# Performance work log

Hardware: AMD Instinct MI355X
Metric: run time of the kernel (lower is better)

## Reference

```python
import jax, jax.numpy as jnp
import numpy as np

MAX_PAGES = 4096
KEY_DIM = 64
PAGE_NUMBER_BITS = 20
BATCH = 32768


def setup_inputs() -> dict:
    key = jax.random.key(0)
    ks = jax.random.split(key, 10)
    return {
        "virtual_page_bits": jax.random.uniform(ks[0], (BATCH, PAGE_NUMBER_BITS), dtype=jnp.float32),
        "page_keys": jax.random.normal(ks[1], (MAX_PAGES, KEY_DIM), dtype=jnp.float32) * 0.1,
        "virtual_pages": jax.random.normal(ks[2], (MAX_PAGES, PAGE_NUMBER_BITS), dtype=jnp.float32) * 0.5,
        "physical_pages": jax.random.normal(ks[3], (MAX_PAGES, PAGE_NUMBER_BITS), dtype=jnp.float32) * 0.5,
        "permissions": jax.random.normal(ks[4], (MAX_PAGES, 4), dtype=jnp.float32) * 0.5,
        "W1": jax.random.normal(ks[5], (PAGE_NUMBER_BITS, 2 * KEY_DIM), dtype=jnp.float32) * 0.1,
        "b1": jnp.zeros((2 * KEY_DIM,), dtype=jnp.float32),
        "W2": jax.random.normal(ks[6], (2 * KEY_DIM, KEY_DIM), dtype=jnp.float32) * 0.1,
        "b2": jnp.zeros((KEY_DIM,), dtype=jnp.float32),
        "temperature": jnp.array(0.5, dtype=jnp.float32),
    }


def reference(virtual_page_bits, page_keys, virtual_pages, physical_pages,
              permissions, W1, b1, W2, b2, temperature):
    # query encoder: Linear -> GELU (exact, torch default) -> Linear
    h = jax.nn.gelu(virtual_page_bits @ W1 + b1, approximate=False)
    query = h @ W2 + b2                                  # [B, key_dim]

    stored_virt = jax.nn.sigmoid(virtual_pages)          # [P, 20]
    key_sim = query @ page_keys.T                        # [B, P]

    x2 = jnp.sum(virtual_page_bits ** 2, axis=-1, keepdims=True)   # [B, 1]
    s2 = jnp.sum(stored_virt ** 2, axis=-1)                        # [P]
    cross = virtual_page_bits @ stored_virt.T                      # [B, P]
    page_sim = -(x2 + s2[None, :] - 2.0 * cross)                   # [B, P]

    combined_sim = key_sim + 2.0 * page_sim
    temp = jnp.maximum(jnp.abs(temperature), 0.1)
    attention = jax.nn.softmax(combined_sim / temp, axis=-1)       # [B, P]

    physical_page_bits = attention @ jax.nn.sigmoid(physical_pages)  # [B, 20]
    perms = attention @ jax.nn.sigmoid(permissions)                  # [B, 4]
    return (physical_page_bits, perms[:, 0], perms[:, 1:4])
```

## Files before the change

### kernel.cpp

```cpp
#include <hip/hip_runtime.h>
#include <hip/hip_bf16.h>
#include <math.h>

typedef __attribute__((ext_vector_type(8))) short short8v;
typedef __attribute__((ext_vector_type(4))) short short4v;
typedef __attribute__((ext_vector_type(4))) float float4v;
typedef unsigned short u16;

#define BATCH 32768
#define PAGES 4096
#define QB 64
#define PT 64
#define NT (PAGES / PT)
#define QS_LD 136

__device__ __forceinline__ u16 f2bf(float f) {
  __hip_bfloat16 h = __float2bfloat16(f);
  union { __hip_bfloat16 h; u16 u; } cv; cv.h = h; return cv.u;
}
__device__ __forceinline__ float bf2f(u16 b) {
  union { u16 u; __hip_bfloat16 h; } cv; cv.u = b; return __bfloat162float(cv.h);
}
__device__ __forceinline__ float sigm(float x) { return 1.0f / (1.0f + __expf(-x)); }

__global__ __launch_bounds__(256) void prep_k(const float* __restrict__ pk,
                                              const float* __restrict__ vp,
                                              u16* __restrict__ Kg,
                                              float* __restrict__ cbg) {
  int tg = blockIdx.x * 256 + threadIdx.x;
  int p = tg >> 4, c = tg & 15;
  short8v vals;
#pragma unroll
  for (int e = 0; e < 8; ++e) {
    int d = c * 8 + e;
    u16 bits;
    if (d < 64) {
      bits = f2bf(pk[p * 64 + d]);
    } else if (d < 124) {
      int j = (d - 64) % 20;
      float s4 = 4.0f * sigm(vp[p * 20 + j]);
      u16 hi = f2bf(s4);
      bits = (d < 104) ? hi : f2bf(s4 - bf2f(hi));
    } else {
      bits = 0;
    }
    vals[e] = (short)bits;
  }
  int cs = c ^ (p & 7);
  *reinterpret_cast<short8v*>(&Kg[p * 128 + cs * 8]) = vals;
  if (c == 0) {
    float s2 = 0.0f;
#pragma unroll
    for (int j = 0; j < 20; ++j) { float s = sigm(vp[p * 20 + j]); s2 += s * s; }
    cbg[p] = -2.0f * s2;
  }
}

__global__ __launch_bounds__(256) void prep_v(const float* __restrict__ ph,
                                              const float* __restrict__ pr,
                                              u16* __restrict__ Vtg) {
  int tg = blockIdx.x * 256 + threadIdx.x;
  int p = tg & 4095, v = tg >> 12;
  float x;
  if (v < 20) x = sigm(ph[p * 20 + v]);
  else if (v < 24) x = sigm(pr[p * 4 + (v - 20)]);
  else x = 0.0f;
  int s = (p & 15) * 4 + ((p >> 4) & 3);
  Vtg[v * 4096 + (p & ~63) + s] = f2bf(x);
}

__global__ __launch_bounds__(256) void mmu_main(
    const float* __restrict__ vpb_g, const float* __restrict__ W1g,
    const float* __restrict__ b1g, const float* __restrict__ W2g,
    const float* __restrict__ b2g, const float* __restrict__ temp_g,
    const u16* __restrict__ Kg, const float* __restrict__ cbg,
    const u16* __restrict__ Vtg, float* __restrict__ outp) {
  __shared__ __align__(16) u16 Qs[QB * QS_LD];
  __shared__ __align__(16) float vpb_s[QB * 20];
  __shared__ __align__(16) char un[26624];
  float* W1s = (float*)un;
  float* hs  = (float*)(un + 10240);
  u16* Ks    = (u16*)un;
  u16* Ps    = (u16*)(un + 16384);

  const int tid = threadIdx.x;
  const int q0 = blockIdx.x * QB;

  for (int i = tid; i < QB * 20; i += 256) vpb_s[i] = vpb_g[q0 * 20 + i];
  for (int i = tid; i < 20 * 128; i += 256) W1s[i] = W1g[i];
  __syncthreads();

  for (int i = tid; i < QB * 64; i += 256) {
    int q = i >> 6, c = 64 + (i & 63);
    u16 bits;
    if (c < 84) bits = f2bf(vpb_s[q * 20 + c - 64]);
    else if (c < 104) { float v = vpb_s[q * 20 + c - 84]; u16 hi = f2bf(v); bits = f2bf(v - bf2f(hi)); }
    else if (c < 124) bits = f2bf(vpb_s[q * 20 + c - 104]);
    else bits = 0;
    Qs[q * QS_LD + c] = bits;
  }

  for (int half = 0; half < 2; ++half) {
    const int qb = half * 32;
    for (int i = tid; i < 32 * 128; i += 256) {
      int q = i >> 7, cc = i & 127;
      float acc = b1g[cc];
#pragma unroll
      for (int j = 0; j < 20; ++j) acc += vpb_s[(qb + q) * 20 + j] * W1s[j * 128 + cc];
      hs[i] = 0.5f * acc * (1.0f + erff(acc * 0.70710678118654752f));
    }
    __syncthreads();
    for (int i = tid; i < 32 * 64; i += 256) {
      int q = i >> 6, k = i & 63;
      float acc = b2g[k];
      for (int c = 0; c < 128; ++c) acc += hs[q * 128 + c] * W2g[c * 64 + k];
      Qs[(qb + q) * QS_LD + k] = f2bf(acc);
    }
    __syncthreads();
  }

  const int lane = tid & 63, w = tid >> 6, g = lane >> 4, li = lane & 15;
  const float invt = 1.0f / fmaxf(fabsf(temp_g[0]), 0.1f);
  const float c2 = invt * 1.4426950408889634f;

  short8v qf[4];
#pragma unroll
  for (int ks = 0; ks < 4; ++ks)
    qf[ks] = *reinterpret_cast<const short8v*>(&Qs[(w * 16 + li) * QS_LD + ks * 32 + g * 8]);

  float4v Ov0 = {0.f, 0.f, 0.f, 0.f}, Ov1 = {0.f, 0.f, 0.f, 0.f};
  float m_run[4] = {-1e30f, -1e30f, -1e30f, -1e30f};
  float lsum[4] = {0.f, 0.f, 0.f, 0.f};
  u16* Psw = Ps + w * (16 * 72);

  for (int t = 0; t < NT; ++t) {
    const short8v* gsrc = reinterpret_cast<const short8v*>(Kg) + t * 1024;
    short8v s0 = gsrc[tid], s1 = gsrc[256 + tid], s2 = gsrc[512 + tid], s3 = gsrc[768 + tid];
    __syncthreads();
    short8v* kdst = reinterpret_cast<short8v*>(Ks);
    kdst[tid] = s0; kdst[256 + tid] = s1; kdst[512 + tid] = s2; kdst[768 + tid] = s3;
    __syncthreads();

    const int p0 = t * PT;
    float sv[4][4];
#pragma unroll
    for (int ct = 0; ct < 4; ++ct) {
      float4v acc = {0.f, 0.f, 0.f, 0.f};
      const int row = ct * 16 + li;
      const float cbv = cbg[p0 + row];
#pragma unroll
      for (int ks = 0; ks < 4; ++ks) {
        const int ch = (ks * 4 + g) ^ (row & 7);
        short8v b = *reinterpret_cast<const short8v*>(&Ks[row * 128 + ch * 8]);
        acc = __builtin_amdgcn_mfma_f32_16x16x32_bf16(qf[ks], b, acc, 0, 0, 0);
      }
#pragma unroll
      for (int r = 0; r < 4; ++r) sv[ct][r] = acc[r] + cbv;
    }

    float mt[4];
#pragma unroll
    for (int r = 0; r < 4; ++r)
      mt[r] = fmaxf(fmaxf(sv[0][r], sv[1][r]), fmaxf(sv[2][r], sv[3][r]));
#pragma unroll
    for (int msk = 1; msk <= 8; msk <<= 1) {
#pragma unroll
      for (int r = 0; r < 4; ++r) mt[r] = fmaxf(mt[r], __shfl_xor(mt[r], msk));
    }
    float fr[4];
#pragma unroll
    for (int r = 0; r < 4; ++r) {
      float mn = fmaxf(m_run[r], mt[r]);
      fr[r] = exp2f((m_run[r] - mn) * c2);
      m_run[r] = mn;
    }
#pragma unroll
    for (int r = 0; r < 4; ++r) {
      const float mc = m_run[r] * c2;
      float p0v = exp2f(sv[0][r] * c2 - mc);
      float p1v = exp2f(sv[1][r] * c2 - mc);
      float p2v = exp2f(sv[2][r] * c2 - mc);
      float p3v = exp2f(sv[3][r] * c2 - mc);
      lsum[r] = lsum[r] * fr[r] + ((p0v + p1v) + (p2v + p3v));
      short4v pb;
      pb[0] = (short)f2bf(p0v); pb[1] = (short)f2bf(p1v);
      pb[2] = (short)f2bf(p2v); pb[3] = (short)f2bf(p3v);
      *reinterpret_cast<short4v*>(&Psw[(g * 4 + r) * 72 + li * 4]) = pb;
    }
#pragma unroll
    for (int r = 0; r < 4; ++r) { Ov0[r] *= fr[r]; Ov1[r] *= fr[r]; }

#pragma unroll
    for (int ks2 = 0; ks2 < 2; ++ks2) {
      short8v a = *reinterpret_cast<const short8v*>(&Psw[li * 72 + ks2 * 32 + g * 8]);
      short8v b0 = *reinterpret_cast<const short8v*>(&Vtg[(li) * 4096 + p0 + ks2 * 32 + g * 8]);
      short8v b1v = *reinterpret_cast<const short8v*>(&Vtg[(16 + li) * 4096 + p0 + ks2 * 32 + g * 8]);
      Ov0 = __builtin_amdgcn_mfma_f32_16x16x32_bf16(a, b0, Ov0, 0, 0, 0);
      Ov1 = __builtin_amdgcn_mfma_f32_16x16x32_bf16(a, b1v, Ov1, 0, 0, 0);
    }
  }

#pragma unroll
  for (int msk = 1; msk <= 8; msk <<= 1) {
#pragma unroll
    for (int r = 0; r < 4; ++r) lsum[r] += __shfl_xor(lsum[r], msk);
  }
#pragma unroll
  for (int r = 0; r < 4; ++r) {
    const float inv = 1.0f / lsum[r];
    const int q = q0 + w * 16 + g * 4 + r;
    outp[q * 20 + li] = Ov0[r] * inv;
    const int vc = 16 + li;
    const float v1 = Ov1[r] * inv;
    if (vc < 20) outp[q * 20 + vc] = v1;
    else if (vc == 20) outp[BATCH * 20 + q] = v1;
    else if (vc < 24) outp[BATCH * 21 + q * 3 + (vc - 21)] = v1;
  }
}

extern "C" void kernel_launch(void* const* d_in, const int* in_sizes, int n_in,
                              void* d_out, int out_size, void* d_ws, size_t ws_size,
                              hipStream_t stream) {
  const float* vpb = (const float*)d_in[0];
  const float* pk  = (const float*)d_in[1];
  const float* vp  = (const float*)d_in[2];
  const float* ph  = (const float*)d_in[3];
  const float* pr  = (const float*)d_in[4];
  const float* W1  = (const float*)d_in[5];
  const float* b1  = (const float*)d_in[6];
  const float* W2  = (const float*)d_in[7];
  const float* b2  = (const float*)d_in[8];
  const float* tp  = (const float*)d_in[9];

  u16* Kg    = (u16*)d_ws;
  float* cbg = (float*)((char*)d_ws + PAGES * 128 * 2);
  u16* Vtg   = (u16*)((char*)d_ws + PAGES * 128 * 2 + PAGES * 4);
  float* outp = (float*)d_out;

  hipLaunchKernelGGL(prep_k, dim3(256), dim3(256), 0, stream, pk, vp, Kg, cbg);
  hipLaunchKernelGGL(prep_v, dim3(512), dim3(256), 0, stream, ph, pr, Vtg);
  hipLaunchKernelGGL(mmu_main, dim3(512), dim3(256), 0, stream,
                     vpb, W1, b1, W2, b2, tp, Kg, cbg, Vtg, outp);
}
```

Before: 252.1 us.

## Double-buffer K tiles via direct-to-LDS loads and widen query block per wave

```diff
diff --git a/kernel.cpp b/kernel.cpp
--- a/kernel.cpp
+++ b/kernel.cpp
@@ -9,9 +9,7 @@
 
 #define BATCH 32768
 #define PAGES 4096
-#define QB 64
-#define PT 64
-#define NT (PAGES / PT)
+#define QB 128
 #define QS_LD 136
 
 __device__ __forceinline__ u16 f2bf(float f) {
@@ -23,68 +21,168 @@
 }
 __device__ __forceinline__ float sigm(float x) { return 1.0f / (1.0f + __expf(-x)); }
 
-__global__ __launch_bounds__(256) void prep_k(const float* __restrict__ pk,
-                                              const float* __restrict__ vp,
-                                              u16* __restrict__ Kg,
-                                              float* __restrict__ cbg) {
-  int tg = blockIdx.x * 256 + threadIdx.x;
-  int p = tg >> 4, c = tg & 15;
-  short8v vals;
-#pragma unroll
-  for (int e = 0; e < 8; ++e) {
-    int d = c * 8 + e;
-    u16 bits;
-    if (d < 64) {
-      bits = f2bf(pk[p * 64 + d]);
-    } else if (d < 124) {
-      int j = (d - 64) % 20;
-      float s4 = 4.0f * sigm(vp[p * 20 + j]);
-      u16 hi = f2bf(s4);
-      bits = (d < 104) ? hi : f2bf(s4 - bf2f(hi));
-    } else {
-      bits = 0;
-    }
-    vals[e] = (short)bits;
-  }
-  int cs = c ^ (p & 7);
-  *reinterpret_cast<short8v*>(&Kg[p * 128 + cs * 8]) = vals;
-  if (c == 0) {
-    float s2 = 0.0f;
-#pragma unroll
-    for (int j = 0; j < 20; ++j) { float s = sigm(vp[p * 20 + j]); s2 += s * s; }
-    cbg[p] = -2.0f * s2;
-  }
-}
-
-__global__ __launch_bounds__(256) void prep_v(const float* __restrict__ ph,
-                                              const float* __restrict__ pr,
-                                              u16* __restrict__ Vtg) {
-  int tg = blockIdx.x * 256 + threadIdx.x;
-  int p = tg & 4095, v = tg >> 12;
-  float x;
-  if (v < 20) x = sigm(ph[p * 20 + v]);
-  else if (v < 24) x = sigm(pr[p * 4 + (v - 20)]);
-  else x = 0.0f;
-  int s = (p & 15) * 4 + ((p >> 4) & 3);
-  Vtg[v * 4096 + (p & ~63) + s] = f2bf(x);
-}
-
-__global__ __launch_bounds__(256) void mmu_main(
+__device__ __forceinline__ void gl_lds16(const void* g, void* l) {
+  __builtin_amdgcn_global_load_lds(
+      (const __attribute__((address_space(1))) unsigned int*)g,
+      (__attribute__((address_space(3))) unsigned int*)l, 16, 0, 0);
+}
+
+__global__ __launch_bounds__(256) void prep(const float* __restrict__ pk,
+                                            const float* __restrict__ vp,
+                                            const float* __restrict__ ph,
+                                            const float* __restrict__ pr,
+                                            u16* __restrict__ Kg,
+                                            u16* __restrict__ Vtg) {
+  if (blockIdx.x < 256) {
+    int tg = blockIdx.x * 256 + threadIdx.x;
+    int p = tg >> 4, c = tg & 15;
+    float cb = 0.0f;
+    if (c == 15) {
+#pragma unroll
+      for (int j = 0; j < 20; ++j) { float s = sigm(vp[p * 20 + j]); cb += s * s; }
+      cb *= -2.0f;
+    }
+    short8v vals;
+#pragma unroll
+    for (int e = 0; e < 8; ++e) {
+      int d = c * 8 + e;
+      u16 bits;
+      if (d < 64) {
+        bits = f2bf(pk[p * 64 + d]);
+      } else if (d < 124) {
+        int j = (d - 64) % 20;
+        float s4 = 4.0f * sigm(vp[p * 20 + j]);
+        u16 hi = f2bf(s4);
+        bits = (d < 104) ? hi : f2bf(s4 - bf2f(hi));
+      } else if (d < 126) {
+        bits = f2bf(cb);
+      } else if (d == 126) {
+        u16 hi = f2bf(cb);
+        bits = f2bf(cb - bf2f(hi));
+      } else {
+        bits = 0;
+      }
+      vals[e] = (short)bits;
+    }
+    int cs = c ^ (p & 7);
+    *reinterpret_cast<short8v*>(&Kg[p * 128 + cs * 8]) = vals;
+  } else {
+    int tg = (blockIdx.x - 256) * 256 + threadIdx.x;
+    int p = tg & 4095, v = tg >> 12;
+    float x;
+    if (v < 20) x = sigm(ph[p * 20 + v]);
+    else if (v < 24) x = sigm(pr[p * 4 + (v - 20)]);
+    else x = 0.0f;
+    int s = (p & 15) * 4 + ((p >> 4) & 3);
+    Vtg[v * 4096 + (p & ~63) + s] = f2bf(x);
+  }
+}
+
+__device__ __forceinline__ void readqk(const u16* __restrict__ Kb,
+                                       const short8v (&qf)[2][4],
+                                       float4v (&A)[2][4], int li, int g) {
+#pragma unroll
+  for (int ct = 0; ct < 4; ++ct) {
+    A[0][ct] = (float4v){0.f, 0.f, 0.f, 0.f};
+    A[1][ct] = (float4v){0.f, 0.f, 0.f, 0.f};
+#pragma unroll
+    for (int ks = 0; ks < 4; ++ks) {
+      short8v b = *reinterpret_cast<const short8v*>(
+          &Kb[(ct * 16 + li) * 128 + (((ks * 4 + g) ^ (li & 7)) << 3)]);
+      A[0][ct] = __builtin_amdgcn_mfma_f32_16x16x32_bf16(qf[0][ks], b, A[0][ct], 0, 0, 0);
+      A[1][ct] = __builtin_amdgcn_mfma_f32_16x16x32_bf16(qf[1][ks], b, A[1][ct], 0, 0, 0);
+    }
+  }
+}
+
+__device__ __forceinline__ void smpv(float4v (&A)[2][4], float (&m_run)[2][4],
+                                     float (&lsum)[2][4], float4v (&Ov)[2][2],
+                                     u16* __restrict__ Psw, const u16* __restrict__ Vtg,
+                                     int tn, int li, int g) {
+  float rmax[2][4];
+#pragma unroll
+  for (int h = 0; h < 2; ++h)
+#pragma unroll
+    for (int r = 0; r < 4; ++r)
+      rmax[h][r] = fmaxf(fmaxf(A[h][0][r], A[h][1][r]), fmaxf(A[h][2][r], A[h][3][r]));
+
+  float d = -1e30f;
+#pragma unroll
+  for (int h = 0; h < 2; ++h)
+#pragma unroll
+    for (int r = 0; r < 4; ++r) d = fmaxf(d, rmax[h][r] - m_run[h][r]);
+
+  if (!__all(d <= 8.0f)) {
+#pragma unroll
+    for (int msk = 1; msk <= 8; msk <<= 1)
+#pragma unroll
+      for (int h = 0; h < 2; ++h)
+#pragma unroll
+        for (int r = 0; r < 4; ++r)
+          rmax[h][r] = fmaxf(rmax[h][r], __shfl_xor(rmax[h][r], msk));
+#pragma unroll
+    for (int h = 0; h < 2; ++h)
+#pragma unroll
+      for (int r = 0; r < 4; ++r) {
+        float mn = fmaxf(m_run[h][r], rmax[h][r]);
+        float fr = exp2f(m_run[h][r] - mn);
+        m_run[h][r] = mn;
+        lsum[h][r] *= fr;
+        Ov[h][0][r] *= fr;
+        Ov[h][1][r] *= fr;
+      }
+  }
+
+#pragma unroll
+  for (int h = 0; h < 2; ++h)
+#pragma unroll
+    for (int r = 0; r < 4; ++r) {
+      const float m = m_run[h][r];
+      float p0 = exp2f(A[h][0][r] - m);
+      float p1 = exp2f(A[h][1][r] - m);
+      float p2 = exp2f(A[h][2][r] - m);
+      float p3 = exp2f(A[h][3][r] - m);
+      lsum[h][r] += (p0 + p1) + (p2 + p3);
+      short4v pb;
+      pb[0] = (short)f2bf(p0); pb[1] = (short)f2bf(p1);
+      pb[2] = (short)f2bf(p2); pb[3] = (short)f2bf(p3);
+      *reinterpret_cast<short4v*>(&Psw[h * 1152 + (g * 4 + r) * 72 + li * 4]) = pb;
+    }
+
+  const u16* vt = Vtg + tn * 64;
+#pragma unroll
+  for (int ks2 = 0; ks2 < 2; ++ks2) {
+    short8v a0 = *reinterpret_cast<const short8v*>(&Psw[0 * 1152 + li * 72 + ks2 * 32 + g * 8]);
+    short8v a1 = *reinterpret_cast<const short8v*>(&Psw[1 * 1152 + li * 72 + ks2 * 32 + g * 8]);
+    short8v b0 = *reinterpret_cast<const short8v*>(&vt[li * 4096 + ks2 * 32 + g * 8]);
+    short8v b1 = *reinterpret_cast<const short8v*>(&vt[(16 + li) * 4096 + ks2 * 32 + g * 8]);
+    Ov[0][0] = __builtin_amdgcn_mfma_f32_16x16x32_bf16(a0, b0, Ov[0][0], 0, 0, 0);
+    Ov[0][1] = __builtin_amdgcn_mfma_f32_16x16x32_bf16(a0, b1, Ov[0][1], 0, 0, 0);
+    Ov[1][0] = __builtin_amdgcn_mfma_f32_16x16x32_bf16(a1, b0, Ov[1][0], 0, 0, 0);
+    Ov[1][1] = __builtin_amdgcn_mfma_f32_16x16x32_bf16(a1, b1, Ov[1][1], 0, 0, 0);
+  }
+}
+
+__global__ __launch_bounds__(256, 1) void mmu_main(
     const float* __restrict__ vpb_g, const float* __restrict__ W1g,
     const float* __restrict__ b1g, const float* __restrict__ W2g,
     const float* __restrict__ b2g, const float* __restrict__ temp_g,
-    const u16* __restrict__ Kg, const float* __restrict__ cbg,
-    const u16* __restrict__ Vtg, float* __restrict__ outp) {
+    const u16* __restrict__ Kg, const u16* __restrict__ Vtg,
+    float* __restrict__ outp) {
+  __shared__ __align__(16) u16 Ks2[2][8192];
   __shared__ __align__(16) u16 Qs[QB * QS_LD];
-  __shared__ __align__(16) float vpb_s[QB * 20];
-  __shared__ __align__(16) char un[26624];
-  float* W1s = (float*)un;
-  float* hs  = (float*)(un + 10240);
-  u16* Ks    = (u16*)un;
-  u16* Ps    = (u16*)(un + 16384);
+  __shared__ __align__(16) char unB[26624];
+  float* W1s = (float*)unB;
+  float* hs  = (float*)(unB + 10240);
+  u16*  Ps   = (u16*)unB;
+  float* vpb_s = (float*)(&Ks2[0][0]);
 
   const int tid = threadIdx.x;
   const int q0 = blockIdx.x * QB;
+  const float invt = 1.0f / fmaxf(fabsf(temp_g[0]), 0.1f);
+  const float c2 = invt * 1.4426950408889634f;
+  const u16 c2h = f2bf(c2);
+  const u16 c2l = f2bf(c2 - bf2f(c2h));
 
   for (int i = tid; i < QB * 20; i += 256) vpb_s[i] = vpb_g[q0 * 20 + i];
   for (int i = tid; i < 20 * 128; i += 256) W1s[i] = W1g[i];
@@ -93,14 +191,16 @@
   for (int i = tid; i < QB * 64; i += 256) {
     int q = i >> 6, c = 64 + (i & 63);
     u16 bits;
-    if (c < 84) bits = f2bf(vpb_s[q * 20 + c - 64]);
-    else if (c < 104) { float v = vpb_s[q * 20 + c - 84]; u16 hi = f2bf(v); bits = f2bf(v - bf2f(hi)); }
-    else if (c < 124) bits = f2bf(vpb_s[q * 20 + c - 104]);
+    if (c < 84) bits = f2bf(c2 * vpb_s[q * 20 + c - 64]);
+    else if (c < 104) { float v = c2 * vpb_s[q * 20 + c - 84]; u16 hi = f2bf(v); bits = f2bf(v - bf2f(hi)); }
+    else if (c < 124) bits = f2bf(c2 * vpb_s[q * 20 + c - 104]);
+    else if (c == 124 || c == 126) bits = c2h;
+    else if (c == 125) bits = c2l;
     else bits = 0;
     Qs[q * QS_LD + c] = bits;
   }
 
-  for (int half = 0; half < 2; ++half) {
+  for (int half = 0; half < 4; ++half) {
     const int qb = half * 32;
     for (int i = tid; i < 32 * 128; i += 256) {
       int q = i >> 7, cc = i & 127;
@@ -114,108 +214,79 @@
       int q = i >> 6, k = i & 63;
       float acc = b2g[k];
       for (int c = 0; c < 128; ++c) acc += hs[q * 128 + c] * W2g[c * 64 + k];
-      Qs[(qb + q) * QS_LD + k] = f2bf(acc);
+      Qs[(qb + q) * QS_LD + k] = f2bf(c2 * acc);
     }
     __syncthreads();
   }
 
   const int lane = tid & 63, w = tid >> 6, g = lane >> 4, li = lane & 15;
-  const float invt = 1.0f / fmaxf(fabsf(temp_g[0]), 0.1f);
-  const float c2 = invt * 1.4426950408889634f;
-
-  short8v qf[4];
-#pragma unroll
-  for (int ks = 0; ks < 4; ++ks)
-    qf[ks] = *reinterpret_cast<const short8v*>(&Qs[(w * 16 + li) * QS_LD + ks * 32 + g * 8]);
-
-  float4v Ov0 = {0.f, 0.f, 0.f, 0.f}, Ov1 = {0.f, 0.f, 0.f, 0.f};
-  float m_run[4] = {-1e30f, -1e30f, -1e30f, -1e30f};
-  float lsum[4] = {0.f, 0.f, 0.f, 0.f};
-  u16* Psw = Ps + w * (16 * 72);
-
-  for (int t = 0; t < NT; ++t) {
-    const short8v* gsrc = reinterpret_cast<const short8v*>(Kg) + t * 1024;
-    short8v s0 = gsrc[tid], s1 = gsrc[256 + tid], s2 = gsrc[512 + tid], s3 = gsrc[768 + tid];
+  u16* Psw = Ps + w * 2304;
+
+  short8v qf[2][4];
+#pragma unroll
+  for (int h = 0; h < 2; ++h)
+#pragma unroll
+    for (int ks = 0; ks < 4; ++ks)
+      qf[h][ks] = *reinterpret_cast<const short8v*>(
+          &Qs[(w * 32 + h * 16 + li) * QS_LD + ks * 32 + g * 8]);
+
+  float4v accA[2][4], accB[2][4];
+  float4v Ov[2][2] = {{{0.f,0.f,0.f,0.f},{0.f,0.f,0.f,0.f}},
+                      {{0.f,0.f,0.f,0.f},{0.f,0.f,0.f,0.f}}};
+  float m_run[2][4] = {{-1e30f,-1e30f,-1e30f,-1e30f},{-1e30f,-1e30f,-1e30f,-1e30f}};
+  float lsum[2][4] = {{0.f,0.f,0.f,0.f},{0.f,0.f,0.f,0.f}};
+
+#define STAGE(tn, sb) {                                                    \
+    const char* gsrc_ = (const char*)Kg + ((size_t)(tn) << 14) + (tid << 4); \
+    u16* ld_ = &Ks2[sb][tid * 8];                                          \
+    gl_lds16(gsrc_,         ld_);                                          \
+    gl_lds16(gsrc_ + 4096,  ld_ + 2048);                                   \
+    gl_lds16(gsrc_ + 8192,  ld_ + 4096);                                   \
+    gl_lds16(gsrc_ + 12288, ld_ + 6144);                                   \
+  }
+
+  STAGE(0, 0);
+  __syncthreads();
+  STAGE(1, 1);
+  readqk(&Ks2[0][0], qf, accA, li, g);
+
+  for (int tt = 0; tt < 62; tt += 2) {
     __syncthreads();
-    short8v* kdst = reinterpret_cast<short8v*>(Ks);
-    kdst[tid] = s0; kdst[256 + tid] = s1; kdst[512 + tid] = s2; kdst[768 + tid] = s3;
+    STAGE(tt + 2, 0);
+    readqk(&Ks2[1][0], qf, accB, li, g);
+    smpv(accA, m_run, lsum, Ov, Psw, Vtg, tt, li, g);
+
     __syncthreads();
-
-    const int p0 = t * PT;
-    float sv[4][4];
-#pragma unroll
-    for (int ct = 0; ct < 4; ++ct) {
-      float4v acc = {0.f, 0.f, 0.f, 0.f};
-      const int row = ct * 16 + li;
-      const float cbv = cbg[p0 + row];
-#pragma unroll
-      for (int ks = 0; ks < 4; ++ks) {
-        const int ch = (ks * 4 + g) ^ (row & 7);
-        short8v b = *reinterpret_cast<const short8v*>(&Ks[row * 128 + ch * 8]);
-        acc = __builtin_amdgcn_mfma_f32_16x16x32_bf16(qf[ks], b, acc, 0, 0, 0);
-      }
-#pragma unroll
-      for (int r = 0; r < 4; ++r) sv[ct][r] = acc[r] + cbv;
-    }
-
-    float mt[4];
-#pragma unroll
-    for (int r = 0; r < 4; ++r)
-      mt[r] = fmaxf(fmaxf(sv[0][r], sv[1][r]), fmaxf(sv[2][r], sv[3][r]));
-#pragma unroll
-    for (int msk = 1; msk <= 8; msk <<= 1) {
-#pragma unroll
-      for (int r = 0; r < 4; ++r) mt[r] = fmaxf(mt[r], __shfl_xor(mt[r], msk));
-    }
-    float fr[4];
+    STAGE(tt + 3, 1);
+    readqk(&Ks2[0][0], qf, accA, li, g);
+    smpv(accB, m_run, lsum, Ov, Psw, Vtg, tt + 1, li, g);
+  }
+  __syncthreads();
+  readqk(&Ks2[1][0], qf, accB, li, g);
+  smpv(accA, m_run, lsum, Ov, Psw, Vtg, 62, li, g);
+  smpv(accB, m_run, lsum, Ov, Psw, Vtg, 63, li, g);
+#undef STAGE
+
+#pragma unroll
+  for (int msk = 1; msk <= 8; msk <<= 1)
+#pragma unroll
+    for (int h = 0; h < 2; ++h)
+#pragma unroll
+      for (int r = 0; r < 4; ++r) lsum[h][r] += __shfl_xor(lsum[h][r], msk);
+
+#pragma unroll
+  for (int h = 0; h < 2; ++h)
 #pragma unroll
     for (int r = 0; r < 4; ++r) {
-      float mn = fmaxf(m_run[r], mt[r]);
-      fr[r] = exp2f((m_run[r] - mn) * c2);
-      m_run[r] = mn;
-    }
-#pragma unroll
-    for (int r = 0; r < 4; ++r) {
-      const float mc = m_run[r] * c2;
-      float p0v = exp2f(sv[0][r] * c2 - mc);
-      float p1v = exp2f(sv[1][r] * c2 - mc);
-      float p2v = exp2f(sv[2][r] * c2 - mc);
-      float p3v = exp2f(sv[3][r] * c2 - mc);
-      lsum[r] = lsum[r] * fr[r] + ((p0v + p1v) + (p2v + p3v));
-      short4v pb;
-      pb[0] = (short)f2bf(p0v); pb[1] = (short)f2bf(p1v);
-      pb[2] = (short)f2bf(p2v); pb[3] = (short)f2bf(p3v);
-      *reinterpret_cast<short4v*>(&Psw[(g * 4 + r) * 72 + li * 4]) = pb;
-    }
-#pragma unroll
-    for (int r = 0; r < 4; ++r) { Ov0[r] *= fr[r]; Ov1[r] *= fr[r]; }
-
-#pragma unroll
-    for (int ks2 = 0; ks2 < 2; ++ks2) {
-      short8v a = *reinterpret_cast<const short8v*>(&Psw[li * 72 + ks2 * 32 + g * 8]);
-      short8v b0 = *reinterpret_cast<const short8v*>(&Vtg[(li) * 4096 + p0 + ks2 * 32 + g * 8]);
-      short8v b1v = *reinterpret_cast<const short8v*>(&Vtg[(16 + li) * 4096 + p0 + ks2 * 32 + g * 8]);
-      Ov0 = __builtin_amdgcn_mfma_f32_16x16x32_bf16(a, b0, Ov0, 0, 0, 0);
-      Ov1 = __builtin_amdgcn_mfma_f32_16x16x32_bf16(a, b1v, Ov1, 0, 0, 0);
-    }
-  }
-
-#pragma unroll
-  for (int msk = 1; msk <= 8; msk <<= 1) {
-#pragma unroll
-    for (int r = 0; r < 4; ++r) lsum[r] += __shfl_xor(lsum[r], msk);
-  }
-#pragma unroll
-  for (int r = 0; r < 4; ++r) {
-    const float inv = 1.0f / lsum[r];
-    const int q = q0 + w * 16 + g * 4 + r;
-    outp[q * 20 + li] = Ov0[r] * inv;
-    const int vc = 16 + li;
-    const float v1 = Ov1[r] * inv;
-    if (vc < 20) outp[q * 20 + vc] = v1;
-    else if (vc == 20) outp[BATCH * 20 + q] = v1;
-    else if (vc < 24) outp[BATCH * 21 + q * 3 + (vc - 21)] = v1;
-  }
+      const float inv = 1.0f / lsum[h][r];
+      const int q = q0 + w * 32 + h * 16 + g * 4 + r;
+      outp[q * 20 + li] = Ov[h][0][r] * inv;
+      const int vc = 16 + li;
+      const float v1 = Ov[h][1][r] * inv;
+      if (vc < 20) outp[q * 20 + vc] = v1;
+      else if (vc == 20) outp[BATCH * 20 + q] = v1;
+      else if (vc < 24) outp[BATCH * 21 + q * 3 + (vc - 21)] = v1;
+    }
 }
 
 extern "C" void kernel_launch(void* const* d_in, const int* in_sizes, int n_in,
@@ -232,13 +303,11 @@
   const float* b2  = (const float*)d_in[8];
   const float* tp  = (const float*)d_in[9];
 
-  u16* Kg    = (u16*)d_ws;
-  float* cbg = (float*)((char*)d_ws + PAGES * 128 * 2);
-  u16* Vtg   = (u16*)((char*)d_ws + PAGES * 128 * 2 + PAGES * 4);
+  u16* Kg  = (u16*)d_ws;
+  u16* Vtg = (u16*)((char*)d_ws + PAGES * 128 * 2);
   float* outp = (float*)d_out;
 
-  hipLaunchKernelGGL(prep_k, dim3(256), dim3(256), 0, stream, pk, vp, Kg, cbg);
-  hipLaunchKernelGGL(prep_v, dim3(512), dim3(256), 0, stream, ph, pr, Vtg);
-  hipLaunchKernelGGL(mmu_main, dim3(512), dim3(256), 0, stream,
-                     vpb, W1, b1, W2, b2, tp, Kg, cbg, Vtg, outp);
-}
+  hipLaunchKernelGGL(prep, dim3(768), dim3(256), 0, stream, pk, vp, ph, pr, Kg, Vtg);
+  hipLaunchKernelGGL(mmu_main, dim3(256), dim3(256), 0, stream,
+                     vpb, W1, b1, W2, b2, tp, Kg, Vtg, outp);
+}
```

Measured after the change: 273.9 us. +8.6%, slower.
